# Performance work log

Measured on AMD Instinct MI355X. Metric: run time of the kernel, lower is better.

Reference implementation:

```python
import math
import jax, jax.numpy as jnp
import numpy as np

N_QO_HEADS = 32
N_KV_HEADS = 8
HEAD_DIM = 128
PAGE = 16          # tokens per cache block
NUM_BLOCKS = 512   # total blocks in KV cache
B = 2              # num sequences
SEQ = 2048         # tokens per sequence (q_len == kv_len, prefill)
T = B * SEQ        # total tokens


def setup_inputs() -> dict:
    key = jax.random.key(0)
    ks = jax.random.split(key, 5)
    query = jax.random.normal(ks[0], (T, N_QO_HEADS * HEAD_DIM), dtype=jnp.float32)
    k_new = jax.random.normal(ks[1], (T, N_KV_HEADS * HEAD_DIM), dtype=jnp.float32)
    v_new = jax.random.normal(ks[2], (T, N_KV_HEADS * HEAD_DIM), dtype=jnp.float32)
    key_cache = jax.random.normal(ks[3], (NUM_BLOCKS, PAGE, N_KV_HEADS, HEAD_DIM), dtype=jnp.float32)
    value_cache = jax.random.normal(ks[4], (NUM_BLOCKS, PAGE, N_KV_HEADS, HEAD_DIM), dtype=jnp.float32)
    nb = SEQ // PAGE
    block_tables = jnp.arange(B * nb, dtype=jnp.int32).reshape(B, nb)
    new_cache_slots = jnp.arange(T, dtype=jnp.int32)  # consistent with block_tables
    return {
        'query': query, 'key': k_new, 'value': v_new,
        'key_cache': key_cache, 'value_cache': value_cache,
        'block_tables': block_tables, 'new_cache_slots': new_cache_slots,
    }


def reference(query, key, value, key_cache, value_cache, block_tables, new_cache_slots):
    T_, _ = query.shape
    q = query.reshape(T_, N_QO_HEADS, HEAD_DIM)
    k_new = key.reshape(T_, N_KV_HEADS, HEAD_DIM)
    v_new = value.reshape(T_, N_KV_HEADS, HEAD_DIM)

    # set_kv_cache: scatter new K/V into the paged cache at new_cache_slots
    kc = key_cache.reshape(NUM_BLOCKS * PAGE, N_KV_HEADS, HEAD_DIM).at[new_cache_slots].set(k_new)
    vc = value_cache.reshape(NUM_BLOCKS * PAGE, N_KV_HEADS, HEAD_DIM).at[new_cache_slots].set(v_new)

    # paged gather: per-sequence token indices from block tables
    nb = block_tables.shape[1]
    idx = (block_tables[:, :, None] * PAGE + jnp.arange(PAGE, dtype=jnp.int32)[None, None, :]).reshape(B, SEQ)
    k = kc[idx]  # [B, S, Hkv, d]
    v = vc[idx]  # [B, S, Hkv, d]

    g = N_QO_HEADS // N_KV_HEADS
    qb = q.reshape(B, SEQ, N_KV_HEADS, g, HEAD_DIM)
    sm_scale = 1.0 / math.sqrt(HEAD_DIM)
    scores = jnp.einsum('bqhgd,bkhd->bhgqk', qb, k) * sm_scale  # [B,Hkv,g,S,S]

    # causal mask (q_len == kv_len so mask is k > q)
    causal = jnp.tril(jnp.ones((SEQ, SEQ), dtype=bool))
    scores = jnp.where(causal, scores, -jnp.inf)
    p = jax.nn.softmax(scores, axis=-1)
    o = jnp.einsum('bhgqk,bkhd->bqhgd', p, v)  # [B,S,Hkv,g,d]
    out = o.reshape(T_, N_QO_HEADS * HEAD_DIM).astype(query.dtype)
    return out
```

## Files before the change

kernel.cpp:

```cpp
#include <hip/hip_runtime.h>
#include <cstdint>

#define HQ 32
#define HKV 8
#define D 128
#define PAGE 16
#define SEQB 2048
#define NB 2
#define NBT (SEQB/PAGE)
#define NSLOTS (512*16)

#define BM 32
#define BN 64

typedef __bf16 bf16;
typedef __bf16 bf16x8 __attribute__((ext_vector_type(8)));
typedef float  f32x4  __attribute__((ext_vector_type(4)));

typedef __attribute__((address_space(3))) uint32_t lds_u32_t;
typedef __attribute__((address_space(1))) uint32_t glb_u32_t;

__device__ __forceinline__ void gload16(const bf16* g, bf16* l) {
    __builtin_amdgcn_global_load_lds((const glb_u32_t*)g, (lds_u32_t*)l, 16, 0, 0);
}

__global__ __launch_bounds__(256) void build_inv(const int* __restrict__ slots,
                                                 int* __restrict__ inv) {
    int t = blockIdx.x * 256 + threadIdx.x;
    if (t < NB * SEQB) inv[slots[t]] = t;
}

__global__ __launch_bounds__(256) void pack_kv(
    const float* __restrict__ knew, const float* __restrict__ vnew,
    const float* __restrict__ kc,   const float* __restrict__ vc,
    const int* __restrict__ btab,   const int* __restrict__ inv,
    bf16* __restrict__ Kp, bf16* __restrict__ Vp)
{
    int gid = blockIdx.x;
    if (gid < 2048) {
        int i   = gid*256 + threadIdx.x;
        int d8  = i & 15;
        int sg  = (i >> 4) & (SEQB - 1);
        int hkv = (i >> 15) & 7;
        int b   = i >> 18;
        int phys = btab[b*NBT + (sg >> 4)] * PAGE + (sg & 15);
        int t    = inv[phys];
        const float* src = (t >= 0 ? knew + (size_t)t * (HKV*D)
                                   : kc   + (size_t)phys * (HKV*D)) + hkv*D + d8*8;
        float4 f0 = *(const float4*)src;
        float4 f1 = *(const float4*)(src + 4);
        bf16x8 o;
        o[0]=(bf16)f0.x; o[1]=(bf16)f0.y; o[2]=(bf16)f0.z; o[3]=(bf16)f0.w;
        o[4]=(bf16)f1.x; o[5]=(bf16)f1.y; o[6]=(bf16)f1.z; o[7]=(bf16)f1.w;
        *(bf16x8*)(Kp + ((size_t)(b*HKV + hkv)*SEQB + sg)*D + d8*8) = o;
    } else {
        int i   = (gid - 2048)*256 + threadIdx.x;
        int d   = i & 127;
        int tg  = (i >> 7) & 255;
        int hkv = (i >> 15) & 7;
        int b   = i >> 18;
        int base = (tg >> 3) * 64 + ((tg >> 2) & 1) * 32 + (tg & 3) * 4;
        bf16x8 o;
        #pragma unroll
        for (int u = 0; u < 8; ++u) {
            int sg   = base + (u & 3) + ((u >> 2) << 4);
            int phys = btab[b*NBT + (sg >> 4)] * PAGE + (sg & 15);
            int t    = inv[phys];
            float v = (t >= 0) ? vnew[(size_t)t * (HKV*D) + hkv*D + d]
                               : vc  [(size_t)phys * (HKV*D) + hkv*D + d];
            o[u] = (bf16)v;
        }
        *(bf16x8*)(Vp + ((size_t)(b*HKV + hkv)*D + d)*SEQB + tg*8) = o;
    }
}

__global__ __launch_bounds__(512, 4) void attn(
    const float* __restrict__ q,
    const bf16* __restrict__ Kp,
    const bf16* __restrict__ Vp,
    float* __restrict__ out)
{
    __shared__ bf16 KT[2][BN * D];
    __shared__ bf16 VT[2][BN * D];

    const int hkv = blockIdx.x & 7;
    const int vq  = blockIdx.x >> 3;
    const int b   = blockIdx.y;

    const int tid  = threadIdx.x;
    const int w    = tid >> 6;
    const int head = w & 3;
    const int half = w >> 2;
    const int lane = tid & 63;
    const int c    = lane & 15;
    const int quad = lane >> 4;
    const int hq   = hkv*4 + head;

    const bf16* Kbase = Kp + (size_t)(b*HKV + hkv) * SEQB * D;
    const bf16* Vbase = Vp + (size_t)(b*HKV + hkv) * (size_t)D * SEQB;

    const float CS = 0.08838834764831845f * 1.4426950408889634f;

    int kgo[2], vgo[2];
    #pragma unroll
    for (int it = 0; it < 2; ++it) {
        int o   = tid + it*512;
        int tok = o >> 4, sl = o & 15;
        int g   = (sl & 8) | ((sl & 7) ^ (tok & 7));
        kgo[it] = tok*D + g*8;
        int d = o >> 3, s2 = o & 7;
        int tg = s2 ^ (d & 7);
        vgo[it] = d*SEQB + tg*8;
    }

    int cur = 0;
    #pragma unroll
    for (int it = 0; it < 2; ++it) gload16(Kbase + kgo[it], &KT[0][(tid + it*512)*8]);
    #pragma unroll
    for (int it = 0; it < 2; ++it) gload16(Vbase + vgo[it], &VT[0][(tid + it*512)*8]);

    #pragma unroll 1
    for (int pass = 0; pass < 2; ++pass) {
        const int qt = pass ? vq : 63 - vq;

        bf16x8 qf[2][4];
        #pragma unroll
        for (int u = 0; u < 2; ++u) {
            const float* qrow = q + (size_t)(b*SEQB + qt*BM + u*16 + c) * (HQ*D) + hq*D;
            #pragma unroll
            for (int kk = 0; kk < 4; ++kk) {
                float4 f0 = *(const float4*)(qrow + kk*32 + quad*8);
                float4 f1 = *(const float4*)(qrow + kk*32 + quad*8 + 4);
                bf16x8 a;
                a[0]=(bf16)(f0.x*CS); a[1]=(bf16)(f0.y*CS); a[2]=(bf16)(f0.z*CS); a[3]=(bf16)(f0.w*CS);
                a[4]=(bf16)(f1.x*CS); a[5]=(bf16)(f1.y*CS); a[6]=(bf16)(f1.z*CS); a[7]=(bf16)(f1.w*CS);
                qf[u][kk] = a;
            }
        }

        float lrun[2];
        f32x4 accO[2][4];
        lrun[0] = 0.f; lrun[1] = 0.f;
        #pragma unroll
        for (int u = 0; u < 2; ++u)
            #pragma unroll
            for (int dt = 0; dt < 4; ++dt) accO[u][dt] = (f32x4){0.f,0.f,0.f,0.f};

        const int jmax  = (qt*BM + BM - 1) >> 6;
        const int qrow0 = qt*BM + c;

        for (int j = 0; j <= jmax; ++j) {
            __syncthreads();

            if (j < jmax) {
                const bf16* kgp = Kbase + (size_t)(j+1)*BN*D;
                const bf16* vgp = Vbase + (j+1)*BN;
                #pragma unroll
                for (int it = 0; it < 2; ++it) gload16(kgp + kgo[it], &KT[cur^1][(tid + it*512)*8]);
                #pragma unroll
                for (int it = 0; it < 2; ++it) gload16(vgp + vgo[it], &VT[cur^1][(tid + it*512)*8]);
            } else if (pass == 0) {
                #pragma unroll
                for (int it = 0; it < 2; ++it) gload16(Kbase + kgo[it], &KT[cur^1][(tid + it*512)*8]);
                #pragma unroll
                for (int it = 0; it < 2; ++it) gload16(Vbase + vgo[it], &VT[cur^1][(tid + it*512)*8]);
            }

            const bf16* Kt = KT[cur];
            const bf16* Vt = VT[cur];
            const int kb0  = j * BN;
            const bool diag = (j == jmax);

            uint32_t pw[2][4][2];
            #pragma unroll
            for (int nt = 0; nt < 4; ++nt) {
                const int tok = nt*16 + c;
                f32x4 s0 = (f32x4){0.f,0.f,0.f,0.f};
                f32x4 s1 = (f32x4){0.f,0.f,0.f,0.f};
                __builtin_amdgcn_s_setprio(1);
                #pragma unroll
                for (int kk = 0; kk < 4; ++kk) {
                    int sl = ((kk & 2) << 2) | (((kk & 1) * 4 + quad) ^ (tok & 7));
                    bf16x8 kb = *(const bf16x8*)(Kt + tok*D + sl*8);
                    s0 = __builtin_amdgcn_mfma_f32_16x16x32_bf16(kb, qf[0][kk], s0, 0, 0, 0);
                    s1 = __builtin_amdgcn_mfma_f32_16x16x32_bf16(kb, qf[1][kk], s1, 0, 0, 0);
                }
                __builtin_amdgcn_s_setprio(0);
                const int tokg = kb0 + nt*16 + quad*4;
                #pragma unroll
                for (int u = 0; u < 2; ++u) {
                    f32x4 sv = u ? s1 : s0;
                    float p0 = __builtin_amdgcn_exp2f(sv[0]);
                    float p1 = __builtin_amdgcn_exp2f(sv[1]);
                    float p2 = __builtin_amdgcn_exp2f(sv[2]);
                    float p3 = __builtin_amdgcn_exp2f(sv[3]);
                    if (diag) {
                        const int qr = qrow0 + u*16;
                        if (tokg     > qr) p0 = 0.0f;
                        if (tokg + 1 > qr) p1 = 0.0f;
                        if (tokg + 2 > qr) p2 = 0.0f;
                        if (tokg + 3 > qr) p3 = 0.0f;
                    }
                    lrun[u] += (p0 + p1) + (p2 + p3);
                    asm("v_cvt_pk_bf16_f32 %0, %1, %2" : "=v"(pw[u][nt][0]) : "v"(p0), "v"(p1));
                    asm("v_cvt_pk_bf16_f32 %0, %1, %2" : "=v"(pw[u][nt][1]) : "v"(p2), "v"(p3));
                }
            }

            union PA { uint32_t w[4]; bf16x8 v; };
            PA pa00, pa01, pa10, pa11;
            pa00.w[0]=pw[0][0][0]; pa00.w[1]=pw[0][0][1]; pa00.w[2]=pw[0][1][0]; pa00.w[3]=pw[0][1][1];
            pa01.w[0]=pw[0][2][0]; pa01.w[1]=pw[0][2][1]; pa01.w[2]=pw[0][3][0]; pa01.w[3]=pw[0][3][1];
            pa10.w[0]=pw[1][0][0]; pa10.w[1]=pw[1][0][1]; pa10.w[2]=pw[1][1][0]; pa10.w[3]=pw[1][1][1];
            pa11.w[0]=pw[1][2][0]; pa11.w[1]=pw[1][2][1]; pa11.w[2]=pw[1][3][0]; pa11.w[3]=pw[1][3][1];
            const int sl0 = ((quad    ) ^ (c & 7)) * 8;
            const int sl1 = ((quad + 4) ^ (c & 7)) * 8;
            __builtin_amdgcn_s_setprio(1);
            #pragma unroll
            for (int dt = 0; dt < 4; ++dt) {
                const bf16* vrow = Vt + (size_t)((half*4 + dt)*16 + c) * BN;
                bf16x8 vb0 = *(const bf16x8*)(vrow + sl0);
                accO[0][dt] = __builtin_amdgcn_mfma_f32_16x16x32_bf16(pa00.v, vb0, accO[0][dt], 0, 0, 0);
                accO[1][dt] = __builtin_amdgcn_mfma_f32_16x16x32_bf16(pa10.v, vb0, accO[1][dt], 0, 0, 0);
                bf16x8 vb1 = *(const bf16x8*)(vrow + sl1);
                accO[0][dt] = __builtin_amdgcn_mfma_f32_16x16x32_bf16(pa01.v, vb1, accO[0][dt], 0, 0, 0);
                accO[1][dt] = __builtin_amdgcn_mfma_f32_16x16x32_bf16(pa11.v, vb1, accO[1][dt], 0, 0, 0);
            }
            __builtin_amdgcn_s_setprio(0);

            cur ^= 1;
        }

        #pragma unroll
        for (int u = 0; u < 2; ++u) {
            float l = lrun[u];
            l += __shfl_xor(l, 16);
            l += __shfl_xor(l, 32);
            #pragma unroll
            for (int rr = 0; rr < 4; ++rr) {
                float lr = __shfl(l, quad*4 + rr);
                float inv = 1.0f / lr;
                float* orow = out + (size_t)(b*SEQB + qt*BM + u*16 + quad*4 + rr) * (HQ*D) + hq*D;
                #pragma unroll
                for (int dt = 0; dt < 4; ++dt)
                    orow[(half*4 + dt)*16 + c] = accO[u][dt][rr] * inv;
            }
        }
    }
}

extern "C" void kernel_launch(void* const* d_in, const int* in_sizes, int n_in,
                              void* d_out, int out_size, void* d_ws, size_t ws_size,
                              hipStream_t stream) {
    const float* q     = (const float*)d_in[0];
    const float* knew  = (const float*)d_in[1];
    const float* vnew  = (const float*)d_in[2];
    const float* kc    = (const float*)d_in[3];
    const float* vc    = (const float*)d_in[4];
    const int*   btab  = (const int*)d_in[5];
    const int*   slots = (const int*)d_in[6];
    float*       out   = (float*)d_out;

    int*  inv = (int*)d_ws;
    bf16* Kp  = (bf16*)((char*)d_ws + 65536);
    bf16* Vp  = Kp + (size_t)NB * HKV * SEQB * D;

    hipMemsetAsync(inv, 0xFF, NSLOTS * sizeof(int), stream);
    build_inv<<<(NB*SEQB + 255)/256, 256, 0, stream>>>(slots, inv);
    pack_kv<<<4096, 256, 0, stream>>>(knew, vnew, kc, vc, btab, inv, Kp, Vp);

    dim3 grid(8 * 32, NB);
    attn<<<grid, 512, 0, stream>>>(q, Kp, Vp, out);
}
```

Baseline: 288.1 us.

## Split key tiles across warp halves and reduce partial outputs through LDS

Previously both warp halves computed the full QK^T scores and softmax exponentials for all four 16-key sub-tiles, and split only the PV product by output dimension. Now each half handles two of the four key sub-tiles and accumulates all 128 output dims. The two halves' partial accumulators and row sums are then combined through LDS scratch, reusing the idle K/V buffer, before normalising and writing out. This removes the duplicated score MFMAs and exp work, but doubles the accumulator registers under launch_bounds(512,4) and adds barriers plus an LDS reduction per pass.

```diff
diff --git a/kernel.cpp b/kernel.cpp
--- a/kernel.cpp
+++ b/kernel.cpp
@@ -82,6 +82,7 @@
 {
     __shared__ bf16 KT[2][BN * D];
     __shared__ bf16 VT[2][BN * D];
+    __shared__ float Ls[4][16];
 
     const int hkv = blockIdx.x & 7;
     const int vq  = blockIdx.x >> 3;
@@ -139,12 +140,12 @@
         }
 
         float lrun[2];
-        f32x4 accO[2][4];
+        f32x4 accO[2][8];
         lrun[0] = 0.f; lrun[1] = 0.f;
         #pragma unroll
         for (int u = 0; u < 2; ++u)
             #pragma unroll
-            for (int dt = 0; dt < 4; ++dt) accO[u][dt] = (f32x4){0.f,0.f,0.f,0.f};
+            for (int dt = 0; dt < 8; ++dt) accO[u][dt] = (f32x4){0.f,0.f,0.f,0.f};
 
         const int jmax  = (qt*BM + BM - 1) >> 6;
         const int qrow0 = qt*BM + c;
@@ -171,9 +172,10 @@
             const int kb0  = j * BN;
             const bool diag = (j == jmax);
 
-            uint32_t pw[2][4][2];
-            #pragma unroll
-            for (int nt = 0; nt < 4; ++nt) {
+            uint32_t pw[2][2][2];
+            #pragma unroll
+            for (int ntl = 0; ntl < 2; ++ntl) {
+                const int nt  = half*2 + ntl;
                 const int tok = nt*16 + c;
                 f32x4 s0 = (f32x4){0.f,0.f,0.f,0.f};
                 f32x4 s1 = (f32x4){0.f,0.f,0.f,0.f};
@@ -202,50 +204,60 @@
                         if (tokg + 3 > qr) p3 = 0.0f;
                     }
                     lrun[u] += (p0 + p1) + (p2 + p3);
-                    asm("v_cvt_pk_bf16_f32 %0, %1, %2" : "=v"(pw[u][nt][0]) : "v"(p0), "v"(p1));
-                    asm("v_cvt_pk_bf16_f32 %0, %1, %2" : "=v"(pw[u][nt][1]) : "v"(p2), "v"(p3));
+                    asm("v_cvt_pk_bf16_f32 %0, %1, %2" : "=v"(pw[u][ntl][0]) : "v"(p0), "v"(p1));
+                    asm("v_cvt_pk_bf16_f32 %0, %1, %2" : "=v"(pw[u][ntl][1]) : "v"(p2), "v"(p3));
                 }
             }
 
             union PA { uint32_t w[4]; bf16x8 v; };
-            PA pa00, pa01, pa10, pa11;
-            pa00.w[0]=pw[0][0][0]; pa00.w[1]=pw[0][0][1]; pa00.w[2]=pw[0][1][0]; pa00.w[3]=pw[0][1][1];
-            pa01.w[0]=pw[0][2][0]; pa01.w[1]=pw[0][2][1]; pa01.w[2]=pw[0][3][0]; pa01.w[3]=pw[0][3][1];
-            pa10.w[0]=pw[1][0][0]; pa10.w[1]=pw[1][0][1]; pa10.w[2]=pw[1][1][0]; pa10.w[3]=pw[1][1][1];
-            pa11.w[0]=pw[1][2][0]; pa11.w[1]=pw[1][2][1]; pa11.w[2]=pw[1][3][0]; pa11.w[3]=pw[1][3][1];
-            const int sl0 = ((quad    ) ^ (c & 7)) * 8;
-            const int sl1 = ((quad + 4) ^ (c & 7)) * 8;
+            PA pa0, pa1;
+            pa0.w[0]=pw[0][0][0]; pa0.w[1]=pw[0][0][1]; pa0.w[2]=pw[0][1][0]; pa0.w[3]=pw[0][1][1];
+            pa1.w[0]=pw[1][0][0]; pa1.w[1]=pw[1][0][1]; pa1.w[2]=pw[1][1][0]; pa1.w[3]=pw[1][1][1];
+            const int sl = ((half*4 + quad) ^ (c & 7)) * 8;
             __builtin_amdgcn_s_setprio(1);
             #pragma unroll
-            for (int dt = 0; dt < 4; ++dt) {
-                const bf16* vrow = Vt + (size_t)((half*4 + dt)*16 + c) * BN;
-                bf16x8 vb0 = *(const bf16x8*)(vrow + sl0);
-                accO[0][dt] = __builtin_amdgcn_mfma_f32_16x16x32_bf16(pa00.v, vb0, accO[0][dt], 0, 0, 0);
-                accO[1][dt] = __builtin_amdgcn_mfma_f32_16x16x32_bf16(pa10.v, vb0, accO[1][dt], 0, 0, 0);
-                bf16x8 vb1 = *(const bf16x8*)(vrow + sl1);
-                accO[0][dt] = __builtin_amdgcn_mfma_f32_16x16x32_bf16(pa01.v, vb1, accO[0][dt], 0, 0, 0);
-                accO[1][dt] = __builtin_amdgcn_mfma_f32_16x16x32_bf16(pa11.v, vb1, accO[1][dt], 0, 0, 0);
+            for (int dt = 0; dt < 8; ++dt) {
+                const bf16* vrow = Vt + (size_t)(dt*16 + c) * BN;
+                bf16x8 vb = *(const bf16x8*)(vrow + sl);
+                accO[0][dt] = __builtin_amdgcn_mfma_f32_16x16x32_bf16(pa0.v, vb, accO[0][dt], 0, 0, 0);
+                accO[1][dt] = __builtin_amdgcn_mfma_f32_16x16x32_bf16(pa1.v, vb, accO[1][dt], 0, 0, 0);
             }
             __builtin_amdgcn_s_setprio(0);
 
             cur ^= 1;
         }
 
-        #pragma unroll
+        float* scr = (head < 2) ? ((float*)&KT[cur^1][0]) + head*(16*128)
+                                : ((float*)&VT[cur^1][0]) + (head-2)*(16*128);
+        #pragma unroll 1
         for (int u = 0; u < 2; ++u) {
             float l = lrun[u];
             l += __shfl_xor(l, 16);
             l += __shfl_xor(l, 32);
-            #pragma unroll
-            for (int rr = 0; rr < 4; ++rr) {
-                float lr = __shfl(l, quad*4 + rr);
-                float inv = 1.0f / lr;
-                float* orow = out + (size_t)(b*SEQB + qt*BM + u*16 + quad*4 + rr) * (HQ*D) + hq*D;
-                #pragma unroll
-                for (int dt = 0; dt < 4; ++dt)
-                    orow[(half*4 + dt)*16 + c] = accO[u][dt][rr] * inv;
-            }
-        }
+            __syncthreads();
+            if (half == 1) {
+                #pragma unroll
+                for (int dt = 0; dt < 8; ++dt)
+                    #pragma unroll
+                    for (int rr = 0; rr < 4; ++rr)
+                        scr[(quad*4 + rr)*128 + dt*16 + c] = accO[u][dt][rr];
+                if (lane < 16) Ls[head][c] = l;
+            }
+            __syncthreads();
+            if (half == 0) {
+                #pragma unroll
+                for (int rr = 0; rr < 4; ++rr) {
+                    float l1  = Ls[head][quad*4 + rr];
+                    float lr  = __shfl(l, quad*4 + rr) + l1;
+                    float inv = 1.0f / lr;
+                    float* orow = out + (size_t)(b*SEQB + qt*BM + u*16 + quad*4 + rr) * (HQ*D) + hq*D;
+                    #pragma unroll
+                    for (int dt = 0; dt < 8; ++dt)
+                        orow[dt*16 + c] = (accO[u][dt][rr] + scr[(quad*4 + rr)*128 + dt*16 + c]) * inv;
+                }
+            }
+        }
+        __syncthreads();
     }
 }
 
```

New measurement: 793.5 us. 175% more time.
